# Kernel tuning notes

Measured on AMD Instinct MI355X. Metric: run time of the kernel, lower is better.

## Reference

```python
import jax, jax.numpy as jnp
import numpy as np

LN_EPS = 1e-5

def _proj(x, w, b):
    # 1x1 conv: x [B,C,H,W], w [O,C], b [O]
    return jnp.einsum('bchw,oc->bohw', x, w) + b[None, :, None, None]

def _layernorm(x, w, b):
    # normalize over last dim
    mu = jnp.mean(x, axis=-1, keepdims=True)
    var = jnp.mean(jnp.square(x - mu), axis=-1, keepdims=True)
    return (x - mu) * jax.lax.rsqrt(var + LN_EPS) * w + b

def setup_inputs() -> dict:
    key = jax.random.key(0)
    ks = jax.random.split(key, 12)
    C = 256
    d = {
        's3': jax.random.normal(ks[0], (2, C, 64, 64), jnp.float32),
        's4': jax.random.normal(ks[1], (2, C, 32, 64), jnp.float32),
        's5': jax.random.normal(ks[2], (2, C, 16, 64), jnp.float32),
        'qw': jax.random.normal(ks[3], (C, C), jnp.float32) * 0.02,
        'qb': jax.random.normal(ks[4], (C,), jnp.float32) * 0.02,
        'kw': jax.random.normal(ks[5], (C, C), jnp.float32) * 0.02,
        'kb': jax.random.normal(ks[6], (C,), jnp.float32) * 0.02,
        'vw': jax.random.normal(ks[7], (C, C), jnp.float32) * 0.02,
        'vb': jax.random.normal(ks[8], (C,), jnp.float32) * 0.02,
        'ow': jax.random.normal(ks[9], (C, C), jnp.float32) * 0.02,
        'ob': jax.random.normal(ks[10], (C,), jnp.float32) * 0.02,
        'ln_w': jnp.ones((C,), jnp.float32),
        'ln_b': jnp.zeros((C,), jnp.float32),
    }
    return d

def reference(s3, s4, s5, qw, qb, kw, kb, vw, vb, ow, ob, ln_w, ln_b):
    B, C, H, W = s3.shape
    num_heads = 8
    head_dim = C // num_heads
    scale = head_dim ** -0.5

    q = _proj(s3, qw, qb).reshape(B, C, H * W)            # [B,C,Nq]
    k4 = _proj(s4, kw, kb).reshape(B, C, -1)
    k5 = _proj(s5, kw, kb).reshape(B, C, -1)
    v4 = _proj(s4, vw, vb).reshape(B, C, -1)
    v5 = _proj(s5, vw, vb).reshape(B, C, -1)
    k = jnp.concatenate([k4, k5], axis=-1)                # [B,C,Nk]
    v = jnp.concatenate([v4, v5], axis=-1)

    # [B,C,N] -> [B,h,N,d]
    def split_heads(t):
        Bn, Cn, N = t.shape
        return t.transpose(0, 2, 1).reshape(Bn, N, num_heads, head_dim).transpose(0, 2, 1, 3)

    qh, kh, vh = split_heads(q), split_heads(k), split_heads(v)
    attn = jnp.einsum('bhqd,bhkd->bhqk', qh, kh) * scale
    attn = jax.nn.softmax(attn, axis=-1)
    out = jnp.einsum('bhqk,bhkd->bhqd', attn, vh)         # [B,h,Nq,d]
    out = out.transpose(0, 2, 1, 3).reshape(B, H * W, C)  # [B,Nq,C]
    out = out.transpose(0, 2, 1).reshape(B, C, H, W)
    out = _proj(out, ow, ob)
    out = s3 + out
    out_flat = out.reshape(B, C, H * W).transpose(0, 2, 1)  # [B,N,C]
    out_flat = _layernorm(out_flat, ln_w, ln_b)
    return out_flat.transpose(0, 2, 1).reshape(B, C, H, W)
```

## Files before the change

### kernel.cpp

```cpp
#include <hip/hip_runtime.h>

typedef __bf16 bf16;
typedef __bf16 bf16x4 __attribute__((ext_vector_type(4)));
typedef __bf16 bf16x8 __attribute__((ext_vector_type(8)));
typedef _Float16 f16;
typedef _Float16 f16x4 __attribute__((ext_vector_type(4)));
typedef float f32x4 __attribute__((ext_vector_type(4)));
typedef unsigned int u32x4 __attribute__((ext_vector_type(4)));

#define MFMA16 __builtin_amdgcn_mfma_f32_16x16x32_bf16
#define MFMA16F __builtin_amdgcn_mfma_f32_16x16x16f16

__device__ __forceinline__ void async16(void* lds, const void* g) {
    __builtin_amdgcn_global_load_lds((const __attribute__((address_space(1))) unsigned int*)g,
                                     (__attribute__((address_space(3))) unsigned int*)lds, 16, 0, 0);
}

__global__ __launch_bounds__(256) void k_prep(const float* __restrict__ qw, const float* __restrict__ kw,
                                              const float* __restrict__ vw, const float* __restrict__ ow,
                                              bf16* __restrict__ Wb,
                                              const float* __restrict__ s3, const float* __restrict__ s4,
                                              const float* __restrict__ s5,
                                              bf16* __restrict__ s3t, bf16* __restrict__ s45t) {
    __shared__ float T[64][65];
    int bx = blockIdx.x, t = threadIdx.x;
    if (bx < 256) {
        int tt = bx * 256 + t;
        const float* srcs[4] = {qw, kw, vw, ow};
        int which = tt >> 14;
        int idx = (tt & 16383) * 4;
        f32x4 v = *(const f32x4*)(srcs[which] + idx);
        bf16x4 o;
        o[0] = (bf16)v[0]; o[1] = (bf16)v[1]; o[2] = (bf16)v[2]; o[3] = (bf16)v[3];
        *(bf16x4*)(Wb + (size_t)which * 65536 + idx) = o;
        return;
    }
    const float* src; bf16* dst; int N, dstRows, rowOff, x, y, z;
    if (bx < 768)       { int i = bx - 256;  src = s3; dst = s3t;  N = 4096; dstRows = 4096; rowOff = 0;    x = i & 63; y = (i >> 6) & 3; z = i >> 8; }
    else if (bx < 1024) { int i = bx - 768;  src = s4; dst = s45t; N = 2048; dstRows = 3072; rowOff = 0;    x = i & 31; y = (i >> 5) & 3; z = i >> 7; }
    else                { int i = bx - 1024; src = s5; dst = s45t; N = 1024; dstRows = 3072; rowOff = 2048; x = i & 15; y = (i >> 4) & 3; z = i >> 6; }
    int c0 = y * 64, n0 = x * 64, b = z;
    const float* s = src + ((size_t)b * 256 + c0) * N + n0;
#pragma unroll
    for (int i = 0; i < 4; i++) {
        int flat = i * 256 + t;
        int row = flat >> 4;
        int col = (flat & 15) * 4;
        f32x4 v = *(const f32x4*)(s + (size_t)row * N + col);
        T[row][col + 0] = v[0]; T[row][col + 1] = v[1];
        T[row][col + 2] = v[2]; T[row][col + 3] = v[3];
    }
    __syncthreads();
#pragma unroll
    for (int i = 0; i < 4; i++) {
        int flat = i * 256 + t;
        int nrow = flat >> 4;
        int c4 = (flat & 15) * 4;
        bf16x4 o;
        o[0] = (bf16)T[c4 + 0][nrow]; o[1] = (bf16)T[c4 + 1][nrow];
        o[2] = (bf16)T[c4 + 2][nrow]; o[3] = (bf16)T[c4 + 3][nrow];
        *(bf16x4*)(dst + ((size_t)(b * dstRows + rowOff + n0 + nrow)) * 256 + c0 + c4) = o;
    }
}

__global__ __launch_bounds__(256) void k_qkv(const bf16* __restrict__ Wb,
                                             const bf16* __restrict__ s3t, const bf16* __restrict__ s45t,
                                             const float* __restrict__ qb, const float* __restrict__ kb,
                                             const float* __restrict__ vb,
                                             bf16* __restrict__ Qb, bf16* __restrict__ Kb,
                                             f16* __restrict__ Vtb, float qscale) {
    int i = blockIdx.x;
    int mode, n0, m0, b, Nrows;
    const bf16 *A, *Bt; const float* bias; float oscale = 1.0f;
    if (i < 512) {
        mode = 0; A = Wb; Bt = s3t; bias = qb; Nrows = 4096; oscale = qscale;
        n0 = (i & 63) * 64; m0 = ((i >> 6) & 3) * 64; b = i >> 8;
    } else if (i < 896) {
        unsigned j = i - 512;
        mode = 0; A = Wb + 65536; Bt = s45t; bias = kb; Nrows = 3072;
        n0 = (j % 48u) * 64; unsigned rr = j / 48u; m0 = (rr & 3) * 64; b = rr >> 2;
    } else {
        unsigned j = i - 896;
        mode = 1; A = Wb + 131072; Bt = s45t; bias = vb; Nrows = 3072;
        n0 = (j % 48u) * 64; unsigned rr = j / 48u; m0 = (rr & 3) * 64; b = rr >> 2;
    }
    __shared__ bf16 As[64 * 40];
    __shared__ bf16 Bs[64 * 40];
    int t = threadIdx.x;
    int w = t >> 6, lane = t & 63;
    int lrow = lane & 15, lk = lane >> 4;
    f32x4 acc[4] = {};
    int r = t >> 2, cc = (t & 3) * 8;
    for (int kc = 0; kc < 256; kc += 32) {
        u32x4 va = *(const u32x4*)(A + (size_t)(m0 + r) * 256 + kc + cc);
        u32x4 vbv = *(const u32x4*)(Bt + ((size_t)b * Nrows + n0 + r) * 256 + kc + cc);
        *(u32x4*)(As + r * 40 + cc) = va;
        *(u32x4*)(Bs + r * 40 + cc) = vbv;
        __syncthreads();
        bf16x8 af = *(const bf16x8*)(As + (w * 16 + lrow) * 40 + lk * 8);
#pragma unroll
        for (int ct = 0; ct < 4; ct++) {
            bf16x8 bfr = *(const bf16x8*)(Bs + (ct * 16 + lrow) * 40 + lk * 8);
            acc[ct] = MFMA16(af, bfr, acc[ct], 0, 0, 0);
        }
        __syncthreads();
    }
    int o0 = m0 + w * 16 + lk * 4;
    f32x4 b4 = *(const f32x4*)(bias + o0);
    int head = o0 >> 5;
#pragma unroll
    for (int ct = 0; ct < 4; ct++) {
        int n = n0 + ct * 16 + lrow;
        if (mode == 0) {
            bf16* Dst = (head, Qb);
            Dst = (oscale == 1.0f && Nrows == 3072) ? Kb : Qb;
            int dd = o0 & 31;
            bf16x4 pv;
#pragma unroll
            for (int j = 0; j < 4; j++) pv[j] = (bf16)((acc[ct][j] + b4[j]) * oscale);
            *(bf16x4*)(Dst + ((size_t)(b * 8 + head) * Nrows + n) * 32 + dd) = pv;
        } else {
#pragma unroll
            for (int j = 0; j < 4; j++) {
                int dd = (o0 & 31) + j;
                int kk = ((dd & 7) << 1) | ((dd >> 3) & 1);
                int u = n & 63, g = u >> 2;
                int col = n0 + ((g ^ kk) << 2) + (u & 3);
                Vtb[((size_t)(b * 8 + head) * 32 + dd) * 3072 + col] = (f16)(acc[ct][j] + b4[j]);
            }
        }
    }
}

__global__ __launch_bounds__(256, 4) void k_attn(const bf16* __restrict__ Q, const bf16* __restrict__ K,
                                                 const f16* __restrict__ Vt,
                                                 float* __restrict__ Opart, float* __restrict__ Lsum) {
    int bh = blockIdx.y;
    int q0 = blockIdx.x * 128;
    int sp = blockIdx.z;
    int kn0 = sp * 1536;
    int t = threadIdx.x, w = t >> 6, lane = t & 63;
    int lrow = lane & 15, lk = lane >> 4;
    __shared__ bf16 Ks[2][64 * 32];
    __shared__ f16 Vs[2][32 * 64];
    const bf16* kbase = K + (size_t)bh * 3072 * 32;
    const f16* vbase = Vt + (size_t)bh * 32 * 3072;
    const bf16* kg = kbase + (size_t)(kn0 + w * 16 + (lane >> 2)) * 32 + (lane & 3) * 8;
    const f16* vg = vbase + (size_t)(w * 8 + (lane >> 3)) * 3072 + kn0 + (lane & 7) * 8;
    const bf16* qrow = Q + ((size_t)bh * 4096 + q0 + w * 32 + lrow) * 32 + lk * 8;
    bf16x8 aq0 = *(const bf16x8*)(qrow);
    bf16x8 aq1 = *(const bf16x8*)(qrow + 16 * 32);
    f16x4 ones;
    ones[0] = (f16)1.f; ones[1] = (f16)1.f; ones[2] = (f16)1.f; ones[3] = (f16)1.f;
    f32x4 accO[2][2] = {};
    f32x4 accL[2] = {};
    f32x4 zero = {};
    int kk2 = ((lrow & 7) << 1) | (lrow >> 3);
    async16(&Ks[0][w * 512], kg);
    async16(&Vs[0][w * 512], vg);
    __syncthreads();
    for (int c = 0; c < 24; ++c) {
        int buf = c & 1;
        if (c < 23) {
            int kc1 = (c + 1) * 64;
            async16(&Ks[buf ^ 1][w * 512], kg + (size_t)kc1 * 32);
            async16(&Vs[buf ^ 1][w * 512], vg + kc1);
        }
        const bf16* ksb = &Ks[buf][0];
        const f16* vsb = &Vs[buf][0];
        f32x4 s0[4], s1[4];
#pragma unroll
        for (int jt = 0; jt < 4; ++jt) {
            bf16x8 kf = *(const bf16x8*)(ksb + (16 * jt + lrow) * 32 + lk * 8);
            s0[jt] = MFMA16(kf, aq0, zero, 0, 0, 0);
            s1[jt] = MFMA16(kf, aq1, zero, 0, 0, 0);
        }
#pragma unroll
        for (int jt = 0; jt < 4; ++jt) {
            f16x4 p0, p1;
#pragma unroll
            for (int i = 0; i < 4; ++i) {
                p0[i] = (f16)__builtin_amdgcn_exp2f(s0[jt][i]);
                p1[i] = (f16)__builtin_amdgcn_exp2f(s1[jt][i]);
            }
            int gcol = (((jt << 2) | lk) ^ kk2) << 2;
            f16x4 vf0 = *(const f16x4*)(vsb + lrow * 64 + gcol);
            f16x4 vf1 = *(const f16x4*)(vsb + (16 + lrow) * 64 + gcol);
            accO[0][0] = MFMA16F(vf0, p0, accO[0][0], 0, 0, 0);
            accO[0][1] = MFMA16F(vf1, p0, accO[0][1], 0, 0, 0);
            accO[1][0] = MFMA16F(vf0, p1, accO[1][0], 0, 0, 0);
            accO[1][1] = MFMA16F(vf1, p1, accO[1][1], 0, 0, 0);
            accL[0] = MFMA16F(ones, p0, accL[0], 0, 0, 0);
            accL[1] = MFMA16F(ones, p1, accL[1], 0, 0, 0);
        }
        __syncthreads();
    }
    int sb = sp * 16 + bh;
    float* Ob = Opart + (size_t)sb * 32 * 4096;
#pragma unroll
    for (int qg = 0; qg < 2; ++qg) {
        int q = q0 + w * 32 + qg * 16 + lrow;
#pragma unroll
        for (int dh = 0; dh < 2; ++dh)
#pragma unroll
            for (int i = 0; i < 4; ++i)
                Ob[(size_t)(dh * 16 + lk * 4 + i) * 4096 + q] = accO[qg][dh][i];
        if (lane < 16) Lsum[(size_t)sb * 4096 + q] = accL[qg][0];
    }
}

__global__ __launch_bounds__(256) void k_oproj(const bf16* __restrict__ A, const float* __restrict__ Opart,
                                               const float* __restrict__ Ls, const float* __restrict__ bias,
                                               float* __restrict__ opre) {
    int i = blockIdx.x;
    int n0 = (i & 63) * 64, m0 = ((i >> 6) & 3) * 64, b = i >> 8;
    __shared__ bf16 As[64 * 40];
    __shared__ bf16 Bs[64 * 40];
    int t = threadIdx.x;
    int w = t >> 6, lane = t & 63;
    int lrow = lane & 15, lk = lane >> 4;
    f32x4 acc[4] = {};
    int r = t >> 2, cc = (t & 3) * 8;
    int q = n0 + r;
    for (int kc = 0; kc < 256; kc += 32) {
        int h = kc >> 5, bh = b * 8 + h;
        u32x4 va = *(const u32x4*)(A + (size_t)(m0 + r) * 256 + kc + cc);
        const float* o1 = Opart + ((size_t)bh * 32 + cc) * 4096 + q;
        const float* o2 = o1 + (size_t)16 * 32 * 4096;
        float l = Ls[(size_t)bh * 4096 + q] + Ls[(size_t)(16 + bh) * 4096 + q];
        float rl = 1.0f / l;
        bf16x8 bb;
#pragma unroll
        for (int u = 0; u < 8; ++u)
            bb[u] = (bf16)((o1[(size_t)u * 4096] + o2[(size_t)u * 4096]) * rl);
        *(u32x4*)(As + r * 40 + cc) = va;
        *(bf16x8*)(Bs + r * 40 + cc) = bb;
        __syncthreads();
        bf16x8 af = *(const bf16x8*)(As + (w * 16 + lrow) * 40 + lk * 8);
#pragma unroll
        for (int ct = 0; ct < 4; ct++) {
            bf16x8 bfr = *(const bf16x8*)(Bs + (ct * 16 + lrow) * 40 + lk * 8);
            acc[ct] = MFMA16(af, bfr, acc[ct], 0, 0, 0);
        }
        __syncthreads();
    }
    int o0 = m0 + w * 16 + lk * 4;
    f32x4 b4 = *(const f32x4*)(bias + o0);
#pragma unroll
    for (int ct = 0; ct < 4; ct++) {
        int n = n0 + ct * 16 + lrow;
        f32x4 v;
#pragma unroll
        for (int j = 0; j < 4; j++) v[j] = acc[ct][j] + b4[j];
        *(f32x4*)(opre + ((size_t)b * 4096 + n) * 256 + o0) = v;
    }
}

__global__ __launch_bounds__(256) void k_ln(const float* __restrict__ opre, const float* __restrict__ s3,
                                            const float* __restrict__ lnw, const float* __restrict__ lnb,
                                            float* __restrict__ out) {
    int b = blockIdx.y;
    int n0 = blockIdx.x * 32;
    __shared__ float T[32][257];
    __shared__ float mu_s[32], rs_s[32];
    int t = threadIdx.x;
#pragma unroll
    for (int i = 0; i < 8; i++) {
        int flat = i * 256 + t;
        int n = flat >> 6;
        int c = (flat & 63) * 4;
        f32x4 v = *(const f32x4*)(opre + ((size_t)b * 4096 + n0 + n) * 256 + c);
        T[n][c + 0] = v[0]; T[n][c + 1] = v[1]; T[n][c + 2] = v[2]; T[n][c + 3] = v[3];
    }
    __syncthreads();
#pragma unroll
    for (int i = 0; i < 8; i++) {
        int flat = i * 256 + t;
        int c = flat >> 3;
        int n = (flat & 7) * 4;
        f32x4 v = *(const f32x4*)(s3 + ((size_t)b * 256 + c) * 4096 + n0 + n);
        T[n + 0][c] += v[0]; T[n + 1][c] += v[1]; T[n + 2][c] += v[2]; T[n + 3][c] += v[3];
    }
    __syncthreads();
    int w = t >> 6, lane = t & 63;
    for (int j = 0; j < 8; j++) {
        int row = w * 8 + j;
        float x0 = T[row][lane], x1 = T[row][lane + 64];
        float x2 = T[row][lane + 128], x3 = T[row][lane + 192];
        float s = x0 + x1 + x2 + x3;
        float s2 = x0 * x0 + x1 * x1 + x2 * x2 + x3 * x3;
#pragma unroll
        for (int off = 1; off < 64; off <<= 1) {
            s += __shfl_xor(s, off, 64);
            s2 += __shfl_xor(s2, off, 64);
        }
        if (lane == 0) {
            float mu = s * (1.0f / 256.0f);
            float var = s2 * (1.0f / 256.0f) - mu * mu;
            mu_s[row] = mu;
            rs_s[row] = rsqrtf(var + 1e-5f);
        }
    }
    __syncthreads();
    int c = t;
    float wv = lnw[c], bv = lnb[c];
#pragma unroll
    for (int i = 0; i < 8; i++) {
        int n = i * 4;
        f32x4 o;
#pragma unroll
        for (int k = 0; k < 4; k++)
            o[k] = (T[n + k][c] - mu_s[n + k]) * rs_s[n + k] * wv + bv;
        *(f32x4*)(out + ((size_t)b * 256 + c) * 4096 + n0 + n) = o;
    }
}

extern "C" void kernel_launch(void* const* d_in, const int* in_sizes, int n_in,
                              void* d_out, int out_size, void* d_ws, size_t ws_size,
                              hipStream_t stream) {
    const float* s3  = (const float*)d_in[0];
    const float* s4  = (const float*)d_in[1];
    const float* s5  = (const float*)d_in[2];
    const float* qw  = (const float*)d_in[3];
    const float* qb  = (const float*)d_in[4];
    const float* kw  = (const float*)d_in[5];
    const float* kb  = (const float*)d_in[6];
    const float* vw  = (const float*)d_in[7];
    const float* vb  = (const float*)d_in[8];
    const float* ow  = (const float*)d_in[9];
    const float* ob  = (const float*)d_in[10];
    const float* lnw = (const float*)d_in[11];
    const float* lnb = (const float*)d_in[12];
    float* out = (float*)d_out;
    char* ws = (char*)d_ws;

    bf16* Wb    = (bf16*)(ws);
    bf16* s3t   = (bf16*)(ws + (512ull << 10));
    bf16* s45t  = (bf16*)(ws + (4608ull << 10));
    bf16* Qb    = (bf16*)(ws + (7680ull << 10));
    bf16* Kb    = Qb + (2ull * 8 * 4096 * 32);
    f16*  Vtb   = (f16*)(Kb + (2ull * 8 * 3072 * 32));
    float* Opart = (float*)(ws + (17920ull << 10));
    float* Lsum  = (float*)(ws + (34304ull << 10));
    float* opre  = (float*)(ws + (512ull << 10));

    const float qscale = 0.17677669529663688f * 1.4426950408889634f;

    k_prep<<<1152, 256, 0, stream>>>(qw, kw, vw, ow, Wb, s3, s4, s5, s3t, s45t);
    k_qkv<<<1280, 256, 0, stream>>>(Wb, s3t, s45t, qb, kb, vb, Qb, Kb, Vtb, qscale);
    k_attn<<<dim3(32, 16, 2), 256, 0, stream>>>(Qb, Kb, Vtb, Opart, Lsum);
    k_oproj<<<512, 256, 0, stream>>>(Wb + 196608, Opart, Lsum, ob, opre);
    k_ln<<<dim3(128, 2), 256, 0, stream>>>(opre, s3, lnw, lnb, out);
}
```

Baseline: 161.9 us.

## Restructure attention with 16x16x32 f16 MFMA, 4-way key split, fp16 partials

The attention kernel now computes 256 queries per block over a 4-way key split. The P·V product uses the 16x16x32 f16 MFMA, with K rows permuted and V columns swizzled so that P packs straight into 8-wide operands. Row sums come from fdot2 instead of an MFMA against ones. Partial outputs are transposed through LDS and stored as fp16 in query-major layout, which cuts the traffic into the output projection. The output projection now sums four fp16 partials per element, which adds reduction work and some precision loss.

```diff
diff --git a/kernel.cpp b/kernel.cpp
--- a/kernel.cpp
+++ b/kernel.cpp
@@ -4,16 +4,29 @@
 typedef __bf16 bf16x4 __attribute__((ext_vector_type(4)));
 typedef __bf16 bf16x8 __attribute__((ext_vector_type(8)));
 typedef _Float16 f16;
-typedef _Float16 f16x4 __attribute__((ext_vector_type(4)));
+typedef _Float16 f16x2 __attribute__((ext_vector_type(2)));
+typedef _Float16 f16x8 __attribute__((ext_vector_type(8)));
 typedef float f32x4 __attribute__((ext_vector_type(4)));
 typedef unsigned int u32x4 __attribute__((ext_vector_type(4)));
 
 #define MFMA16 __builtin_amdgcn_mfma_f32_16x16x32_bf16
-#define MFMA16F __builtin_amdgcn_mfma_f32_16x16x16f16
+#define MFMA16H __builtin_amdgcn_mfma_f32_16x16x32_f16
 
 __device__ __forceinline__ void async16(void* lds, const void* g) {
     __builtin_amdgcn_global_load_lds((const __attribute__((address_space(1))) unsigned int*)g,
                                      (__attribute__((address_space(3))) unsigned int*)lds, 16, 0, 0);
+}
+
+__device__ __forceinline__ f16x2 pkrtz(float a, float b) {
+    return __builtin_bit_cast(f16x2, __builtin_amdgcn_cvt_pkrtz(a, b));
+}
+
+__device__ __forceinline__ float fdot2h(f16x2 a, f16x2 b, float c) {
+#if __has_builtin(__builtin_amdgcn_fdot2)
+    return __builtin_amdgcn_fdot2(a, b, c, false);
+#else
+    return c + (float)a[0] * (float)b[0] + (float)a[1] * (float)b[1];
+#endif
 }
 
 __global__ __launch_bounds__(256) void k_prep(const float* __restrict__ qw, const float* __restrict__ kw,
@@ -77,11 +90,11 @@
         n0 = (i & 63) * 64; m0 = ((i >> 6) & 3) * 64; b = i >> 8;
     } else if (i < 896) {
         unsigned j = i - 512;
-        mode = 0; A = Wb + 65536; Bt = s45t; bias = kb; Nrows = 3072;
+        mode = 1; A = Wb + 65536; Bt = s45t; bias = kb; Nrows = 3072;
         n0 = (j % 48u) * 64; unsigned rr = j / 48u; m0 = (rr & 3) * 64; b = rr >> 2;
     } else {
         unsigned j = i - 896;
-        mode = 1; A = Wb + 131072; Bt = s45t; bias = vb; Nrows = 3072;
+        mode = 2; A = Wb + 131072; Bt = s45t; bias = vb; Nrows = 3072;
         n0 = (j % 48u) * 64; unsigned rr = j / 48u; m0 = (rr & 3) * 64; b = rr >> 2;
     }
     __shared__ bf16 As[64 * 40];
@@ -112,20 +125,25 @@
     for (int ct = 0; ct < 4; ct++) {
         int n = n0 + ct * 16 + lrow;
         if (mode == 0) {
-            bf16* Dst = (head, Qb);
-            Dst = (oscale == 1.0f && Nrows == 3072) ? Kb : Qb;
             int dd = o0 & 31;
             bf16x4 pv;
 #pragma unroll
             for (int j = 0; j < 4; j++) pv[j] = (bf16)((acc[ct][j] + b4[j]) * oscale);
-            *(bf16x4*)(Dst + ((size_t)(b * 8 + head) * Nrows + n) * 32 + dd) = pv;
+            *(bf16x4*)(Qb + ((size_t)(b * 8 + head) * 4096 + n) * 32 + dd) = pv;
+        } else if (mode == 1) {
+            int dd = o0 & 31;
+            int u = n & 31;
+            int np = (n & ~31) | (((u >> 2) & 1) << 4) | ((u >> 3) << 2) | (u & 3);
+            bf16x4 pv;
+#pragma unroll
+            for (int j = 0; j < 4; j++) pv[j] = (bf16)(acc[ct][j] + b4[j]);
+            *(bf16x4*)(Kb + ((size_t)(b * 8 + head) * 3072 + np) * 32 + dd) = pv;
         } else {
+            int g = (n & 63) >> 3;
 #pragma unroll
             for (int j = 0; j < 4; j++) {
                 int dd = (o0 & 31) + j;
-                int kk = ((dd & 7) << 1) | ((dd >> 3) & 1);
-                int u = n & 63, g = u >> 2;
-                int col = n0 + ((g ^ kk) << 2) + (u & 3);
+                int col = (n & ~63) + ((g ^ (dd & 7)) << 3) + (n & 7);
                 Vtb[((size_t)(b * 8 + head) * 32 + dd) * 3072 + col] = (f16)(acc[ct][j] + b4[j]);
             }
         }
@@ -134,82 +152,105 @@
 
 __global__ __launch_bounds__(256, 4) void k_attn(const bf16* __restrict__ Q, const bf16* __restrict__ K,
                                                  const f16* __restrict__ Vt,
-                                                 float* __restrict__ Opart, float* __restrict__ Lsum) {
+                                                 f16* __restrict__ Opart, float* __restrict__ Lsum) {
     int bh = blockIdx.y;
-    int q0 = blockIdx.x * 128;
+    int q0 = blockIdx.x * 256;
     int sp = blockIdx.z;
-    int kn0 = sp * 1536;
+    int kn0 = sp * 768;
     int t = threadIdx.x, w = t >> 6, lane = t & 63;
     int lrow = lane & 15, lk = lane >> 4;
     __shared__ bf16 Ks[2][64 * 32];
     __shared__ f16 Vs[2][32 * 64];
+    __shared__ f16 Tq[4][32 * 66];
     const bf16* kbase = K + (size_t)bh * 3072 * 32;
     const f16* vbase = Vt + (size_t)bh * 32 * 3072;
     const bf16* kg = kbase + (size_t)(kn0 + w * 16 + (lane >> 2)) * 32 + (lane & 3) * 8;
     const f16* vg = vbase + (size_t)(w * 8 + (lane >> 3)) * 3072 + kn0 + (lane & 7) * 8;
-    const bf16* qrow = Q + ((size_t)bh * 4096 + q0 + w * 32 + lrow) * 32 + lk * 8;
-    bf16x8 aq0 = *(const bf16x8*)(qrow);
-    bf16x8 aq1 = *(const bf16x8*)(qrow + 16 * 32);
-    f16x4 ones;
-    ones[0] = (f16)1.f; ones[1] = (f16)1.f; ones[2] = (f16)1.f; ones[3] = (f16)1.f;
-    f32x4 accO[2][2] = {};
-    f32x4 accL[2] = {};
+    bf16x8 aq[4];
+#pragma unroll
+    for (int qg = 0; qg < 4; ++qg)
+        aq[qg] = *(const bf16x8*)(Q + ((size_t)bh * 4096 + q0 + w * 64 + qg * 16 + lrow) * 32 + lk * 8);
+    f32x4 accO[4][2] = {};
+    float lsum[4] = {0.f, 0.f, 0.f, 0.f};
     f32x4 zero = {};
-    int kk2 = ((lrow & 7) << 1) | (lrow >> 3);
+    f16x2 one2; one2[0] = (f16)1.f; one2[1] = (f16)1.f;
+    int vkey = lrow & 7;
     async16(&Ks[0][w * 512], kg);
     async16(&Vs[0][w * 512], vg);
     __syncthreads();
-    for (int c = 0; c < 24; ++c) {
+    for (int c = 0; c < 12; ++c) {
         int buf = c & 1;
-        if (c < 23) {
-            int kc1 = (c + 1) * 64;
-            async16(&Ks[buf ^ 1][w * 512], kg + (size_t)kc1 * 32);
-            async16(&Vs[buf ^ 1][w * 512], vg + kc1);
+        if (c < 11) {
+            async16(&Ks[buf ^ 1][w * 512], kg + (size_t)(c + 1) * 64 * 32);
+            async16(&Vs[buf ^ 1][w * 512], vg + (c + 1) * 64);
         }
         const bf16* ksb = &Ks[buf][0];
         const f16* vsb = &Vs[buf][0];
-        f32x4 s0[4], s1[4];
-#pragma unroll
-        for (int jt = 0; jt < 4; ++jt) {
-            bf16x8 kf = *(const bf16x8*)(ksb + (16 * jt + lrow) * 32 + lk * 8);
-            s0[jt] = MFMA16(kf, aq0, zero, 0, 0, 0);
-            s1[jt] = MFMA16(kf, aq1, zero, 0, 0, 0);
-        }
-#pragma unroll
-        for (int jt = 0; jt < 4; ++jt) {
-            f16x4 p0, p1;
-#pragma unroll
-            for (int i = 0; i < 4; ++i) {
-                p0[i] = (f16)__builtin_amdgcn_exp2f(s0[jt][i]);
-                p1[i] = (f16)__builtin_amdgcn_exp2f(s1[jt][i]);
+#pragma unroll
+        for (int p = 0; p < 2; ++p) {
+            f32x4 s[2][4];
+#pragma unroll
+            for (int t2 = 0; t2 < 2; ++t2) {
+                bf16x8 kf = *(const bf16x8*)(ksb + (p * 32 + t2 * 16 + lrow) * 32 + lk * 8);
+#pragma unroll
+                for (int qg = 0; qg < 4; ++qg) s[t2][qg] = MFMA16(kf, aq[qg], zero, 0, 0, 0);
             }
-            int gcol = (((jt << 2) | lk) ^ kk2) << 2;
-            f16x4 vf0 = *(const f16x4*)(vsb + lrow * 64 + gcol);
-            f16x4 vf1 = *(const f16x4*)(vsb + (16 + lrow) * 64 + gcol);
-            accO[0][0] = MFMA16F(vf0, p0, accO[0][0], 0, 0, 0);
-            accO[0][1] = MFMA16F(vf1, p0, accO[0][1], 0, 0, 0);
-            accO[1][0] = MFMA16F(vf0, p1, accO[1][0], 0, 0, 0);
-            accO[1][1] = MFMA16F(vf1, p1, accO[1][1], 0, 0, 0);
-            accL[0] = MFMA16F(ones, p0, accL[0], 0, 0, 0);
-            accL[1] = MFMA16F(ones, p1, accL[1], 0, 0, 0);
+            f16x8 p8[4];
+#pragma unroll
+            for (int qg = 0; qg < 4; ++qg) {
+                f16x2 h0 = pkrtz(__builtin_amdgcn_exp2f(s[0][qg][0]), __builtin_amdgcn_exp2f(s[0][qg][1]));
+                f16x2 h1 = pkrtz(__builtin_amdgcn_exp2f(s[0][qg][2]), __builtin_amdgcn_exp2f(s[0][qg][3]));
+                f16x2 h2 = pkrtz(__builtin_amdgcn_exp2f(s[1][qg][0]), __builtin_amdgcn_exp2f(s[1][qg][1]));
+                f16x2 h3 = pkrtz(__builtin_amdgcn_exp2f(s[1][qg][2]), __builtin_amdgcn_exp2f(s[1][qg][3]));
+                f16x8 pk;
+                pk[0] = h0[0]; pk[1] = h0[1]; pk[2] = h1[0]; pk[3] = h1[1];
+                pk[4] = h2[0]; pk[5] = h2[1]; pk[6] = h3[0]; pk[7] = h3[1];
+                p8[qg] = pk;
+                lsum[qg] = fdot2h(h0, one2, lsum[qg]);
+                lsum[qg] = fdot2h(h1, one2, lsum[qg]);
+                lsum[qg] = fdot2h(h2, one2, lsum[qg]);
+                lsum[qg] = fdot2h(h3, one2, lsum[qg]);
+            }
+#pragma unroll
+            for (int dh = 0; dh < 2; ++dh) {
+                f16x8 vf = *(const f16x8*)(vsb + (dh * 16 + lrow) * 64 + ((((p << 2) | lk) ^ vkey) << 3));
+#pragma unroll
+                for (int qg = 0; qg < 4; ++qg)
+                    accO[qg][dh] = MFMA16H(vf, p8[qg], accO[qg][dh], 0, 0, 0);
+            }
         }
         __syncthreads();
     }
     int sb = sp * 16 + bh;
-    float* Ob = Opart + (size_t)sb * 32 * 4096;
-#pragma unroll
-    for (int qg = 0; qg < 2; ++qg) {
-        int q = q0 + w * 32 + qg * 16 + lrow;
+#pragma unroll
+    for (int qg = 0; qg < 4; ++qg) {
+        lsum[qg] += __shfl_xor(lsum[qg], 16, 64);
+        lsum[qg] += __shfl_xor(lsum[qg], 32, 64);
+    }
+    if (lane < 16) {
+#pragma unroll
+        for (int qg = 0; qg < 4; ++qg)
+            Lsum[(size_t)sb * 4096 + q0 + w * 64 + qg * 16 + lane] = lsum[qg];
+    }
+    f16* tw = &Tq[w][0];
+#pragma unroll
+    for (int qg = 0; qg < 4; ++qg)
 #pragma unroll
         for (int dh = 0; dh < 2; ++dh)
 #pragma unroll
             for (int i = 0; i < 4; ++i)
-                Ob[(size_t)(dh * 16 + lk * 4 + i) * 4096 + q] = accO[qg][dh][i];
-        if (lane < 16) Lsum[(size_t)sb * 4096 + q] = accL[qg][0];
-    }
-}
-
-__global__ __launch_bounds__(256) void k_oproj(const bf16* __restrict__ A, const float* __restrict__ Opart,
+                tw[(dh * 16 + lk * 4 + i) * 66 + qg * 16 + lrow] = (f16)accO[qg][dh][i];
+    int q4 = (lane & 15) * 4, dgrp = (lane >> 4) * 8;
+#pragma unroll
+    for (int qq = 0; qq < 4; ++qq) {
+        f16x8 ov;
+#pragma unroll
+        for (int dj = 0; dj < 8; ++dj) ov[dj] = tw[(dgrp + dj) * 66 + q4 + qq];
+        *(f16x8*)(Opart + ((size_t)sb * 4096 + q0 + w * 64 + q4 + qq) * 32 + dgrp) = ov;
+    }
+}
+
+__global__ __launch_bounds__(256) void k_oproj(const bf16* __restrict__ A, const f16* __restrict__ Opart,
                                                const float* __restrict__ Ls, const float* __restrict__ bias,
                                                float* __restrict__ opre) {
     int i = blockIdx.x;
@@ -222,17 +263,22 @@
     f32x4 acc[4] = {};
     int r = t >> 2, cc = (t & 3) * 8;
     int q = n0 + r;
+    const size_t SPS = (size_t)16 * 4096 * 32;
     for (int kc = 0; kc < 256; kc += 32) {
-        int h = kc >> 5, bh = b * 8 + h;
+        int bh = b * 8 + (kc >> 5);
         u32x4 va = *(const u32x4*)(A + (size_t)(m0 + r) * 256 + kc + cc);
-        const float* o1 = Opart + ((size_t)bh * 32 + cc) * 4096 + q;
-        const float* o2 = o1 + (size_t)16 * 32 * 4096;
-        float l = Ls[(size_t)bh * 4096 + q] + Ls[(size_t)(16 + bh) * 4096 + q];
+        float l = Ls[(size_t)bh * 4096 + q] + Ls[(size_t)(16 + bh) * 4096 + q] +
+                  Ls[(size_t)(32 + bh) * 4096 + q] + Ls[(size_t)(48 + bh) * 4096 + q];
         float rl = 1.0f / l;
+        const f16* ob = Opart + ((size_t)bh * 4096 + q) * 32 + cc;
+        f16x8 a0 = *(const f16x8*)(ob);
+        f16x8 a1 = *(const f16x8*)(ob + SPS);
+        f16x8 a2 = *(const f16x8*)(ob + 2 * SPS);
+        f16x8 a3 = *(const f16x8*)(ob + 3 * SPS);
         bf16x8 bb;
 #pragma unroll
-        for (int u = 0; u < 8; ++u)
-            bb[u] = (bf16)((o1[(size_t)u * 4096] + o2[(size_t)u * 4096]) * rl);
+        for (int j = 0; j < 8; ++j)
+            bb[j] = (bf16)((((float)a0[j] + (float)a1[j]) + ((float)a2[j] + (float)a3[j])) * rl);
         *(u32x4*)(As + r * 40 + cc) = va;
         *(bf16x8*)(Bs + r * 40 + cc) = bb;
         __syncthreads();
@@ -340,15 +386,15 @@
     bf16* Qb    = (bf16*)(ws + (7680ull << 10));
     bf16* Kb    = Qb + (2ull * 8 * 4096 * 32);
     f16*  Vtb   = (f16*)(Kb + (2ull * 8 * 3072 * 32));
-    float* Opart = (float*)(ws + (17920ull << 10));
-    float* Lsum  = (float*)(ws + (34304ull << 10));
-    float* opre  = (float*)(ws + (512ull << 10));
+    f16*  Opart = (f16*)(ws + (17920ull << 10));
+    float* Lsum = (float*)(ws + (34304ull << 10));
+    float* opre = (float*)(ws + (512ull << 10));
 
     const float qscale = 0.17677669529663688f * 1.4426950408889634f;
 
     k_prep<<<1152, 256, 0, stream>>>(qw, kw, vw, ow, Wb, s3, s4, s5, s3t, s45t);
     k_qkv<<<1280, 256, 0, stream>>>(Wb, s3t, s45t, qb, kb, vb, Qb, Kb, Vtb, qscale);
-    k_attn<<<dim3(32, 16, 2), 256, 0, stream>>>(Qb, Kb, Vtb, Opart, Lsum);
+    k_attn<<<dim3(16, 16, 4), 256, 0, stream>>>(Qb, Kb, Vtb, Opart, Lsum);
     k_oproj<<<512, 256, 0, stream>>>(Wb + 196608, Opart, Lsum, ob, opre);
     k_ln<<<dim3(128, 2), 256, 0, stream>>>(opre, s3, lnw, lnb, out);
 }
```

After: 154.7 us. 4.4% less time.
